# Kernel tuning notes

Measured on AMD Instinct MI355X. Metric: run time of the kernel, lower is better.

Reference implementation:

```python
import jax, jax.numpy as jnp
from jax import lax
import numpy as np

B, T, I, H, OUT = 4096, 168, 4, 64, 12


def setup_inputs() -> dict:
    key = jax.random.key(0)
    ks = jax.random.split(key, 14)
    s = 0.05
    return {
        "x": jax.random.normal(ks[0], (B, T, I), dtype=jnp.float32),
        # LSTM layer 0 (PyTorch gate order: i, f, g, o)
        "Wih0": jax.random.normal(ks[1], (4 * H, I), dtype=jnp.float32) * s,
        "Whh0": jax.random.normal(ks[2], (4 * H, H), dtype=jnp.float32) * s,
        "bih0": jax.random.normal(ks[3], (4 * H,), dtype=jnp.float32) * s,
        "bhh0": jax.random.normal(ks[4], (4 * H,), dtype=jnp.float32) * s,
        # LSTM layer 1
        "Wih1": jax.random.normal(ks[5], (4 * H, H), dtype=jnp.float32) * s,
        "Whh1": jax.random.normal(ks[6], (4 * H, H), dtype=jnp.float32) * s,
        "bih1": jax.random.normal(ks[7], (4 * H,), dtype=jnp.float32) * s,
        "bhh1": jax.random.normal(ks[8], (4 * H,), dtype=jnp.float32) * s,
        # FC head: Linear(64,64) -> ReLU -> Linear(64,12)
        "W1": jax.random.normal(ks[9], (64, H), dtype=jnp.float32) * s,
        "b1": jax.random.normal(ks[10], (64,), dtype=jnp.float32) * s,
        "W2": jax.random.normal(ks[11], (OUT, 64), dtype=jnp.float32) * s,
        "b2": jax.random.normal(ks[12], (OUT,), dtype=jnp.float32) * s,
    }


def _lstm_layer(x, Wih, Whh, bih, bhh):
    # x: [B, T, in]; returns hidden sequence [B, T, H]
    Bsz = x.shape[0]
    Hd = Whh.shape[1]
    # Precompute input contribution for all timesteps: [B, T, 4H]
    xg = jnp.einsum('bti,gi->btg', x, Wih) + bih + bhh

    def step(carry, xg_t):
        h, c = carry
        g = xg_t + h @ Whh.T  # [B, 4H]
        i, f, gg, o = jnp.split(g, 4, axis=-1)
        i = jax.nn.sigmoid(i)
        f = jax.nn.sigmoid(f)
        gg = jnp.tanh(gg)
        o = jax.nn.sigmoid(o)
        c = f * c + i * gg
        h = o * jnp.tanh(c)
        return (h, c), h

    h0 = jnp.zeros((Bsz, Hd), x.dtype)
    (_, _), hs = lax.scan(step, (h0, h0), jnp.swapaxes(xg, 0, 1))  # hs: [T, B, H]
    return jnp.swapaxes(hs, 0, 1)


def reference(x, Wih0, Whh0, bih0, bhh0, Wih1, Whh1, bih1, bhh1, W1, b1, W2, b2):
    # Eval-mode forward: dropout layers are identity.
    h1 = _lstm_layer(x, Wih0, Whh0, bih0, bhh0)   # [B, T, H]
    h2 = _lstm_layer(h1, Wih1, Whh1, bih1, bhh1)  # [B, T, H]
    last = h2[:, -1, :]                            # [B, H]
    z = jax.nn.relu(last @ W1.T + b1)              # [B, 64]
    out = z @ W2.T + b2                            # [B, 12]
    return out.reshape(-1, 3, 4)
```

## Files before the change

kernel.cpp:

```cpp
#include <hip/hip_runtime.h>


typedef _Float16 h8 __attribute__((ext_vector_type(8)));
typedef _Float16 h4 __attribute__((ext_vector_type(4)));
typedef float f4 __attribute__((ext_vector_type(4)));

#define ROWB 208
#define HBUF (16 * ROWB)
#define XTAB_OFF 0
#define XTAB_BYTES (169 * 256)
#define H0_OFF XTAB_BYTES
#define H1_OFF (H0_OFF + 2 * HBUF)
#define SMEM_TOTAL (H1_OFF + 2 * HBUF)

#define K1F 1.4426950408889634f
#define K2F 2.8853900817779268f

__device__ __forceinline__ float exp2_(float x) {
#if __has_builtin(__builtin_amdgcn_exp2f)
  return __builtin_amdgcn_exp2f(x);
#else
  float r; asm("v_exp_f32 %0, %1" : "=v"(r) : "v"(x)); return r;
#endif
}
__device__ __forceinline__ float rcp_(float x) {
#if __has_builtin(__builtin_amdgcn_rcpf)
  return __builtin_amdgcn_rcpf(x);
#else
  float r; asm("v_rcp_f32 %0, %1" : "=v"(r) : "v"(x)); return r;
#endif
}

__device__ __forceinline__ f4 mfma16(h8 a, h8 b, f4 c) {
  return __builtin_amdgcn_mfma_f32_16x16x32_f16(a, b, c, 0, 0, 0);
}

__device__ __forceinline__ h8 load_w8s(const float* __restrict__ p, float sc) {
  h8 r;
#pragma unroll
  for (int j = 0; j < 8; j++) r[j] = (_Float16)(p[j] * sc);
  return r;
}

__device__ __forceinline__ unsigned packh2(float a, float b) {
  unsigned lo = (unsigned)__builtin_bit_cast(unsigned short, (_Float16)a);
  unsigned hi = (unsigned)__builtin_bit_cast(unsigned short, (_Float16)b);
  return lo | (hi << 16);
}

__device__ __forceinline__ void lstm_act(f4 a, float& c, float& h) {
  float Ei = exp2_(-a[0]);
  float Ef = exp2_(-a[1]);
  float Eg = exp2_(a[2]);
  float Eo = exp2_(-a[3]);
  float A = 1.f + Ei, B = 1.f + Ef, C = 1.f + Eg, D = 1.f + Eo;
  float AB = A * B, CD = C * D;
  float R = rcp_(AB * CD);
  float iv = (B * CD) * R;
  float fv = (A * CD) * R;
  float gv = 1.f - 2.f * ((AB * D) * R);
  float ov = (AB * C) * R;
  c = fv * c + iv * gv;
  float Ec = exp2_(c * K2F);
  h = ov * (1.f - 2.f * rcp_(Ec + 1.f));
}

extern "C" __global__ void __launch_bounds__(512, 1)
weather_lstm_mfma4(const float* __restrict__ x,
                   const float* __restrict__ Wih0, const float* __restrict__ Whh0,
                   const float* __restrict__ bih0, const float* __restrict__ bhh0,
                   const float* __restrict__ Wih1, const float* __restrict__ Whh1,
                   const float* __restrict__ bih1, const float* __restrict__ bhh1,
                   const float* __restrict__ W1, const float* __restrict__ b1,
                   const float* __restrict__ W2, const float* __restrict__ b2,
                   float* __restrict__ out)
{
  __shared__ __align__(16) unsigned char smem[SMEM_TOTAL];
  const int tid  = threadIdx.x;
  const int lane = tid & 63;
  const int w    = tid >> 6;
  const int col  = lane & 15;
  const int quad = lane >> 4;
  const int sB   = blockIdx.x * 16;

  const int g_  = col & 3;
  const int ul_ = col >> 2;
  const float asc = (g_ == 2) ? K2F : K1F;
  int arow[2];
  arow[0] = g_ * 64 + w * 8 + 2 * ul_ + 0;
  arow[1] = g_ * 64 + w * 8 + 2 * ul_ + 1;

  h8 a0[2][3], a1i[2][2], a1h[2][2];
#pragma unroll
  for (int T = 0; T < 2; T++) {
    const int r = arow[T];
#pragma unroll
    for (int f = 0; f < 2; f++) {
      a0[T][f]  = load_w8s(Whh0 + r * 64 + f * 32 + quad * 8, asc);
      a1i[T][f] = load_w8s(Wih1 + r * 64 + f * 32 + quad * 8, asc);
      a1h[T][f] = load_w8s(Whh1 + r * 64 + f * 32 + quad * 8, asc);
    }
    h8 xw = {};
    if (quad == 0) {
#pragma unroll
      for (int j = 0; j < 4; j++) xw[j] = (_Float16)(Wih0[r * 4 + j] * asc);
    }
    a0[T][2] = xw;
  }

  f4 bias0v[2], bias1v[2];
#pragma unroll
  for (int T = 0; T < 2; T++) {
#pragma unroll
    for (int reg = 0; reg < 4; reg++) {
      const int rr = reg * 64 + w * 8 + 2 * quad + T;
      const float bs = (reg == 2) ? K2F : K1F;
      bias0v[T][reg] = (bih0[rr] + bhh0[rr]) * bs;
      bias1v[T][reg] = (bih1[rr] + bhh1[rr]) * bs;
    }
  }

  for (int idx = tid; idx < SMEM_TOTAL / 4; idx += 512) ((int*)smem)[idx] = 0;
  __syncthreads();
  for (int idx = tid; idx < 16 * 168; idx += 512) {
    const int c_ = idx / 168, t_ = idx - c_ * 168;
    f4 xv = *(const f4*)(x + ((size_t)(sB + c_) * 168 + t_) * 4);
    h4 xh;
#pragma unroll
    for (int j = 0; j < 4; j++) xh[j] = (_Float16)xv[j];
    *(h4*)(smem + XTAB_OFF + t_ * 256 + c_ * 16) = xh;
  }
  __syncthreads();

  float c0[2] = {0.f, 0.f}, c1[2] = {0.f, 0.f};
  float hl[2] = {0.f, 0.f};
  const int bo = col * ROWB + quad * 16;
  const int wo = col * ROWB + (w * 8 + 2 * quad) * 2;
  const unsigned char* xp = smem + XTAB_OFF + col * 16;

  for (int k = 0; k <= 168; k++) {
    const int kb = k & 1, kbn = kb ^ 1;
    const unsigned char* h0r = smem + H0_OFF + kbn * HBUF;
    unsigned char*       h0w = smem + H0_OFF + kb  * HBUF;
    const unsigned char* h1r = smem + H1_OFF + kb  * HBUF;
    unsigned char*       h1w = smem + H1_OFF + kbn * HBUF;

    h8 b0  = *(const h8*)(h0r + bo);
    h8 b1v = *(const h8*)(h0r + bo + 64);
    h8 bx  = *(const h8*)(xp + k * 256);
    h8 q0  = *(const h8*)(h1r + bo);
    h8 q1  = *(const h8*)(h1r + bo + 64);

    f4 A0 = mfma16(a0[0][0], b0, bias0v[0]);
    f4 A1 = mfma16(a0[1][0], b0, bias0v[1]);
    f4 C0 = mfma16(a1i[0][0], b0, bias1v[0]);
    f4 C1 = mfma16(a1i[1][0], b0, bias1v[1]);
    A0 = mfma16(a0[0][1], b1v, A0);
    A1 = mfma16(a0[1][1], b1v, A1);
    C0 = mfma16(a1i[0][1], b1v, C0);
    C1 = mfma16(a1i[1][1], b1v, C1);
    A0 = mfma16(a0[0][2], bx, A0);
    A1 = mfma16(a0[1][2], bx, A1);
    C0 = mfma16(a1h[0][0], q0, C0);
    C1 = mfma16(a1h[1][0], q0, C1);
    C0 = mfma16(a1h[0][1], q1, C0);
    C1 = mfma16(a1h[1][1], q1, C1);

    if (k < 168) {
      float h0o[2];
      lstm_act(A0, c0[0], h0o[0]);
      lstm_act(A1, c0[1], h0o[1]);
      *(unsigned*)(h0w + wo) = packh2(h0o[0], h0o[1]);
    }
    if (k > 0) {
      lstm_act(C0, c1[0], hl[0]);
      lstm_act(C1, c1[1], hl[1]);
      *(unsigned*)(h1w + wo) = packh2(hl[0], hl[1]);
    }
    __syncthreads();
  }

  float* fh = (float*)smem;
#pragma unroll
  for (int T = 0; T < 2; T++)
    fh[col * 64 + (w * 8 + 2 * quad + T)] = hl[T];
  __syncthreads();

  {
    const int u = tid & 63, grp = tid >> 6;
    float za0 = b1[u], za1 = b1[u];
    const float* w1r = W1 + u * 64;
    const float* f0 = fh + (grp * 2 + 0) * 64;
    const float* f1 = fh + (grp * 2 + 1) * 64;
    for (int j = 0; j < 64; j++) {
      float wv = w1r[j];
      za0 += wv * f0[j];
      za1 += wv * f1[j];
    }
    float* zl = (float*)(smem + 4096);
    zl[(grp * 2 + 0) * 64 + u] = fmaxf(za0, 0.f);
    zl[(grp * 2 + 1) * 64 + u] = fmaxf(za1, 0.f);
  }
  __syncthreads();

  if (tid < 192) {
    const float* zl = (const float*)(smem + 4096);
    const int s = tid / 12, o = tid - s * 12;
    float a = b2[o];
    for (int j = 0; j < 64; j++) a += W2[o * 64 + j] * zl[s * 64 + j];
    out[(sB + s) * 12 + o] = a;
  }
}

extern "C" void kernel_launch(void* const* d_in, const int* in_sizes, int n_in,
                              void* d_out, int out_size, void* d_ws, size_t ws_size,
                              hipStream_t stream) {
  (void)in_sizes; (void)n_in; (void)d_ws; (void)ws_size; (void)out_size;
  const float* x    = (const float*)d_in[0];
  const float* Wih0 = (const float*)d_in[1];
  const float* Whh0 = (const float*)d_in[2];
  const float* bih0 = (const float*)d_in[3];
  const float* bhh0 = (const float*)d_in[4];
  const float* Wih1 = (const float*)d_in[5];
  const float* Whh1 = (const float*)d_in[6];
  const float* bih1 = (const float*)d_in[7];
  const float* bhh1 = (const float*)d_in[8];
  const float* W1   = (const float*)d_in[9];
  const float* b1   = (const float*)d_in[10];
  const float* W2   = (const float*)d_in[11];
  const float* b2   = (const float*)d_in[12];

  weather_lstm_mfma4<<<dim3(256), dim3(512), 0, stream>>>(
      x, Wih0, Whh0, bih0, bhh0, Wih1, Whh1, bih1, bhh1, W1, b1, W2, b2,
      (float*)d_out);
}
```

Before: 227.0 us.

## Split LSTM gate tiles across 16 waves with one tile per wave

Doubles the block from 512 to 1024 threads so each of 16 waves owns one 16-row gate tile per layer instead of two. The per-step MFMA chain and activation work per wave is halved, shortening the serial critical path of each timestep. It also trims the activation math by folding the input-gate product into one expression. The trade-off is a barrier across twice as many waves every timestep, and half-word LDS stores replacing packed stores.

```diff
diff --git a/kernel.cpp b/kernel.cpp
--- a/kernel.cpp
+++ b/kernel.cpp
@@ -42,31 +42,24 @@
   return r;
 }
 
-__device__ __forceinline__ unsigned packh2(float a, float b) {
-  unsigned lo = (unsigned)__builtin_bit_cast(unsigned short, (_Float16)a);
-  unsigned hi = (unsigned)__builtin_bit_cast(unsigned short, (_Float16)b);
-  return lo | (hi << 16);
-}
-
 __device__ __forceinline__ void lstm_act(f4 a, float& c, float& h) {
   float Ei = exp2_(-a[0]);
   float Ef = exp2_(-a[1]);
   float Eg = exp2_(a[2]);
   float Eo = exp2_(-a[3]);
   float A = 1.f + Ei, B = 1.f + Ef, C = 1.f + Eg, D = 1.f + Eo;
-  float AB = A * B, CD = C * D;
-  float R = rcp_(AB * CD);
-  float iv = (B * CD) * R;
+  float AB = A * B, CD = C * D, BD = B * D;
+  float R  = rcp_(AB * CD);
   float fv = (A * CD) * R;
-  float gv = 1.f - 2.f * ((AB * D) * R);
+  float ig = (BD * (Eg - 1.f)) * R;
   float ov = (AB * C) * R;
-  c = fv * c + iv * gv;
-  float Ec = exp2_(c * K2F);
-  h = ov * (1.f - 2.f * rcp_(Ec + 1.f));
-}
-
-extern "C" __global__ void __launch_bounds__(512, 1)
-weather_lstm_mfma4(const float* __restrict__ x,
+  c = fv * c + ig;
+  float r2 = rcp_(exp2_(c * K2F) + 1.f);
+  h = ov * (1.f - 2.f * r2);
+}
+
+extern "C" __global__ void __launch_bounds__(1024, 4)
+weather_lstm_mfma5(const float* __restrict__ x,
                    const float* __restrict__ Wih0, const float* __restrict__ Whh0,
                    const float* __restrict__ bih0, const float* __restrict__ bhh0,
                    const float* __restrict__ Wih1, const float* __restrict__ Whh1,
@@ -86,43 +79,36 @@
   const int g_  = col & 3;
   const int ul_ = col >> 2;
   const float asc = (g_ == 2) ? K2F : K1F;
-  int arow[2];
-  arow[0] = g_ * 64 + w * 8 + 2 * ul_ + 0;
-  arow[1] = g_ * 64 + w * 8 + 2 * ul_ + 1;
-
-  h8 a0[2][3], a1i[2][2], a1h[2][2];
-#pragma unroll
-  for (int T = 0; T < 2; T++) {
-    const int r = arow[T];
-#pragma unroll
-    for (int f = 0; f < 2; f++) {
-      a0[T][f]  = load_w8s(Whh0 + r * 64 + f * 32 + quad * 8, asc);
-      a1i[T][f] = load_w8s(Wih1 + r * 64 + f * 32 + quad * 8, asc);
-      a1h[T][f] = load_w8s(Whh1 + r * 64 + f * 32 + quad * 8, asc);
-    }
+  const int r = g_ * 64 + w * 4 + ul_;
+
+  h8 a0[3], a1i[2], a1h[2];
+#pragma unroll
+  for (int f = 0; f < 2; f++) {
+    a0[f]  = load_w8s(Whh0 + r * 64 + f * 32 + quad * 8, asc);
+    a1i[f] = load_w8s(Wih1 + r * 64 + f * 32 + quad * 8, asc);
+    a1h[f] = load_w8s(Whh1 + r * 64 + f * 32 + quad * 8, asc);
+  }
+  {
     h8 xw = {};
     if (quad == 0) {
 #pragma unroll
       for (int j = 0; j < 4; j++) xw[j] = (_Float16)(Wih0[r * 4 + j] * asc);
     }
-    a0[T][2] = xw;
-  }
-
-  f4 bias0v[2], bias1v[2];
-#pragma unroll
-  for (int T = 0; T < 2; T++) {
-#pragma unroll
-    for (int reg = 0; reg < 4; reg++) {
-      const int rr = reg * 64 + w * 8 + 2 * quad + T;
-      const float bs = (reg == 2) ? K2F : K1F;
-      bias0v[T][reg] = (bih0[rr] + bhh0[rr]) * bs;
-      bias1v[T][reg] = (bih1[rr] + bhh1[rr]) * bs;
-    }
-  }
-
-  for (int idx = tid; idx < SMEM_TOTAL / 4; idx += 512) ((int*)smem)[idx] = 0;
-  __syncthreads();
-  for (int idx = tid; idx < 16 * 168; idx += 512) {
+    a0[2] = xw;
+  }
+
+  f4 bias0v, bias1v;
+#pragma unroll
+  for (int reg = 0; reg < 4; reg++) {
+    const int rr = reg * 64 + w * 4 + quad;
+    const float bs = (reg == 2) ? K2F : K1F;
+    bias0v[reg] = (bih0[rr] + bhh0[rr]) * bs;
+    bias1v[reg] = (bih1[rr] + bhh1[rr]) * bs;
+  }
+
+  for (int idx = tid; idx < SMEM_TOTAL / 4; idx += 1024) ((int*)smem)[idx] = 0;
+  __syncthreads();
+  for (int idx = tid; idx < 16 * 168; idx += 1024) {
     const int c_ = idx / 168, t_ = idx - c_ * 168;
     f4 xv = *(const f4*)(x + ((size_t)(sB + c_) * 168 + t_) * 4);
     h4 xh;
@@ -132,10 +118,9 @@
   }
   __syncthreads();
 
-  float c0[2] = {0.f, 0.f}, c1[2] = {0.f, 0.f};
-  float hl[2] = {0.f, 0.f};
+  float c0 = 0.f, c1 = 0.f, hl = 0.f;
   const int bo = col * ROWB + quad * 16;
-  const int wo = col * ROWB + (w * 8 + 2 * quad) * 2;
+  const int wo = col * ROWB + (w * 4 + quad) * 2;
   const unsigned char* xp = smem + XTAB_OFF + col * 16;
 
   for (int k = 0; k <= 168; k++) {
@@ -151,55 +136,38 @@
     h8 q0  = *(const h8*)(h1r + bo);
     h8 q1  = *(const h8*)(h1r + bo + 64);
 
-    f4 A0 = mfma16(a0[0][0], b0, bias0v[0]);
-    f4 A1 = mfma16(a0[1][0], b0, bias0v[1]);
-    f4 C0 = mfma16(a1i[0][0], b0, bias1v[0]);
-    f4 C1 = mfma16(a1i[1][0], b0, bias1v[1]);
-    A0 = mfma16(a0[0][1], b1v, A0);
-    A1 = mfma16(a0[1][1], b1v, A1);
-    C0 = mfma16(a1i[0][1], b1v, C0);
-    C1 = mfma16(a1i[1][1], b1v, C1);
-    A0 = mfma16(a0[0][2], bx, A0);
-    A1 = mfma16(a0[1][2], bx, A1);
-    C0 = mfma16(a1h[0][0], q0, C0);
-    C1 = mfma16(a1h[1][0], q0, C1);
-    C0 = mfma16(a1h[0][1], q1, C0);
-    C1 = mfma16(a1h[1][1], q1, C1);
+    f4 A0 = mfma16(a0[0], b0, bias0v);
+    f4 C0 = mfma16(a1i[0], b0, bias1v);
+    A0 = mfma16(a0[1], b1v, A0);
+    C0 = mfma16(a1i[1], b1v, C0);
+    A0 = mfma16(a0[2], bx, A0);
+    C0 = mfma16(a1h[0], q0, C0);
+    C0 = mfma16(a1h[1], q1, C0);
 
     if (k < 168) {
-      float h0o[2];
-      lstm_act(A0, c0[0], h0o[0]);
-      lstm_act(A1, c0[1], h0o[1]);
-      *(unsigned*)(h0w + wo) = packh2(h0o[0], h0o[1]);
+      float h0o;
+      lstm_act(A0, c0, h0o);
+      *(_Float16*)(h0w + wo) = (_Float16)h0o;
     }
     if (k > 0) {
-      lstm_act(C0, c1[0], hl[0]);
-      lstm_act(C1, c1[1], hl[1]);
-      *(unsigned*)(h1w + wo) = packh2(hl[0], hl[1]);
+      lstm_act(C0, c1, hl);
+      *(_Float16*)(h1w + wo) = (_Float16)hl;
     }
     __syncthreads();
   }
 
   float* fh = (float*)smem;
-#pragma unroll
-  for (int T = 0; T < 2; T++)
-    fh[col * 64 + (w * 8 + 2 * quad + T)] = hl[T];
+  fh[col * 64 + (w * 4 + quad)] = hl;
   __syncthreads();
 
   {
     const int u = tid & 63, grp = tid >> 6;
-    float za0 = b1[u], za1 = b1[u];
+    float za = b1[u];
     const float* w1r = W1 + u * 64;
-    const float* f0 = fh + (grp * 2 + 0) * 64;
-    const float* f1 = fh + (grp * 2 + 1) * 64;
-    for (int j = 0; j < 64; j++) {
-      float wv = w1r[j];
-      za0 += wv * f0[j];
-      za1 += wv * f1[j];
-    }
+    const float* f0 = fh + grp * 64;
+    for (int j = 0; j < 64; j++) za += w1r[j] * f0[j];
     float* zl = (float*)(smem + 4096);
-    zl[(grp * 2 + 0) * 64 + u] = fmaxf(za0, 0.f);
-    zl[(grp * 2 + 1) * 64 + u] = fmaxf(za1, 0.f);
+    zl[grp * 64 + u] = fmaxf(za, 0.f);
   }
   __syncthreads();
 
@@ -230,7 +198,7 @@
   const float* W2   = (const float*)d_in[11];
   const float* b2   = (const float*)d_in[12];
 
-  weather_lstm_mfma4<<<dim3(256), dim3(512), 0, stream>>>(
+  weather_lstm_mfma5<<<dim3(256), dim3(1024), 0, stream>>>(
       x, Wih0, Whh0, bih0, bhh0, Wih1, Whh1, bih1, bhh1, W1, b1, W2, b2,
       (float*)d_out);
 }
```

After: 225.5 us. No clear change (-0.6%).
